# Optimization experiments

Hardware: AMD Instinct MI355X
Metric: run time of the kernel (lower is better)

Reference implementation:

```python
import jax, jax.numpy as jnp
import numpy as np
from functools import reduce
from itertools import combinations_with_replacement

ORDER = 2  # Volterra order (matches init_kwargs)


def setup_inputs() -> dict:
    key = jax.random.key(0)
    kx, ka, kw, kb = jax.random.split(key, 4)
    N, D, P = 8192, 256, 3  # nodes, feature dim (in_dim == out_dim), num adjacency powers
    X = jax.random.normal(kx, (N, D), dtype=jnp.float32)
    # dense adjacency powers, scaled so A @ X stays O(1)
    A = jax.random.normal(ka, (P, N, N), dtype=jnp.float32) / np.float32(np.sqrt(N))
    # projective_layers: order+1 Linear(in_dim, out_dim) -> stacked weights/biases
    W = jax.random.normal(kw, (ORDER + 1, D, D), dtype=jnp.float32) / np.float32(np.sqrt(D))
    b = jax.random.normal(kb, (ORDER + 1, D), dtype=jnp.float32) * np.float32(0.01)
    return {"X": X, "A": A, "W": W, "b": b}


def reference(X, A, W, b):
    P = A.shape[0]
    # mat_muls[p] = A_p @ X  -> [P, N, in_dim]
    mat_muls = jnp.einsum('pnm,md->pnd', A, X)
    # order-0 term: Linear_0(X)
    out = X @ W[0].T + b[0]
    for r in range(1, ORDER + 1):
        combos = list(combinations_with_replacement(range(P), r))
        # sum of Hadamard products over all index combinations of size r
        S = reduce(jnp.add,
                   [reduce(jnp.multiply, [mat_muls[i] for i in combo]) for combo in combos])
        # Linear_r applied per combination == (sum of products) @ W_r^T, but the
        # bias is added once PER combination in the original loop.
        out = out + S @ W[r].T + np.float32(len(combos)) * b[r]
    return jax.nn.relu(out)
```

## Files before the change

kernel.cpp:

```cpp
#include <hip/hip_runtime.h>
#include <stdint.h>

typedef __bf16 bf16x8 __attribute__((ext_vector_type(8)));
typedef float floatx4 __attribute__((ext_vector_type(4)));

#define MFMA16(a, b, c) __builtin_amdgcn_mfma_f32_16x16x32_bf16((a), (b), (c), 0, 0, 0)

__device__ __forceinline__ uint32_t pack2bf(float a, float b) {
  uint32_t ua = __builtin_bit_cast(uint32_t, a);
  uint32_t ub = __builtin_bit_cast(uint32_t, b);
  ua = (ua + 0x7fffu + ((ua >> 16) & 1u)) >> 16;
  ub = (ub + 0x7fffu + ((ub >> 16) & 1u)) >> 16;
  return ua | (ub << 16);
}

#define NN 8192
#define DD 256
#define PP 3

__global__ __launch_bounds__(256) void k_transpose_x(const float* __restrict__ X,
                                                     uint16_t* __restrict__ XT) {
  __shared__ float lds[32][260];
  const int n0 = blockIdx.x * 32;
  const int t = threadIdx.x;
#pragma unroll
  for (int j = 0; j < 8; ++j) {
    int idx = t + 256 * j;
    int n = idx >> 6;
    int c = (idx & 63) << 2;
    float4 v = *(const float4*)(X + (size_t)(n0 + n) * DD + c);
    lds[n][c] = v.x; lds[n][c + 1] = v.y; lds[n][c + 2] = v.z; lds[n][c + 3] = v.w;
  }
  __syncthreads();
  const int d = t;
  uint32_t w[16];
#pragma unroll
  for (int i = 0; i < 16; ++i) w[i] = pack2bf(lds[2 * i][d], lds[2 * i + 1][d]);
  uint4* dst = (uint4*)(XT + (size_t)d * NN + n0);
  dst[0] = make_uint4(w[0], w[1], w[2], w[3]);
  dst[1] = make_uint4(w[4], w[5], w[6], w[7]);
  dst[2] = make_uint4(w[8], w[9], w[10], w[11]);
  dst[3] = make_uint4(w[12], w[13], w[14], w[15]);
}

__global__ __launch_bounds__(256) void k_build_wcat(const float* __restrict__ W,
                                                    uint16_t* __restrict__ WcatT) {
  int idx = blockIdx.x * 256 + threadIdx.x;
  int o = idx * 4;
  int d = o / 768;
  int c = o - d * 768;
  int r = c >> 8;
  int e = c & 255;
  float4 v = *(const float4*)(W + (size_t)r * DD * DD + (size_t)d * DD + e);
  *(uint2*)(WcatT + o) = make_uint2(pack2bf(v.x, v.y), pack2bf(v.z, v.w));
}

__global__ __launch_bounds__(256) void k_gemm_ax(const float* __restrict__ A,
                                                 const uint16_t* __restrict__ XT,
                                                 float* __restrict__ M) {
  __shared__ uint16_t ldsA[4 * 64 * 8];
  __shared__ uint16_t ldsB[16 * 64 * 8];

  const int t = threadIdx.x;
  const int lane = t & 63;
  const int wid = t >> 6;
  const int wm = wid >> 1;
  const int wn = wid & 1;
  const int rt = blockIdx.x;
  const int p = blockIdx.y;

  const float* Ap = A + (size_t)p * NN * NN + (size_t)rt * 64 * NN;
  float* Mp = M + (size_t)p * NN * DD;

  const int arow = t >> 2;
  const int aq = t & 3;
  const float* aptr = Ap + (size_t)arow * NN + aq * 8;
  const int alds = (((arow >> 4) * 64) + ((aq << 4) | (arow & 15))) * 8;

  const uint16_t* xptr0;
  const uint16_t* xptr1;
  const uint16_t* xptr2;
  const uint16_t* xptr3;
  int xlds[4];
  {
    const uint16_t* tmp[4];
#pragma unroll
    for (int j = 0; j < 4; ++j) {
      int idx = t + 256 * j;
      int nl = idx >> 2;
      int q = idx & 3;
      tmp[j] = XT + (size_t)nl * NN + q * 8;
      xlds[j] = (((nl >> 4) * 64) + ((q << 4) | (nl & 15))) * 8;
    }
    xptr0 = tmp[0]; xptr1 = tmp[1]; xptr2 = tmp[2]; xptr3 = tmp[3];
  }

  floatx4 acc[2][8];
#pragma unroll
  for (int i = 0; i < 2; ++i)
#pragma unroll
    for (int j = 0; j < 8; ++j) acc[i][j] = (floatx4){0.f, 0.f, 0.f, 0.f};

  for (int k0 = 0; k0 < NN; k0 += 32) {
    float4 a0 = *(const float4*)(aptr);
    float4 a1 = *(const float4*)(aptr + 4);
    aptr += 32;
    uint4 xv0 = *(const uint4*)xptr0; xptr0 += 32;
    uint4 xv1 = *(const uint4*)xptr1; xptr1 += 32;
    uint4 xv2 = *(const uint4*)xptr2; xptr2 += 32;
    uint4 xv3 = *(const uint4*)xptr3; xptr3 += 32;

    __syncthreads();
    uint4 apk;
    apk.x = pack2bf(a0.x, a0.y);
    apk.y = pack2bf(a0.z, a0.w);
    apk.z = pack2bf(a1.x, a1.y);
    apk.w = pack2bf(a1.z, a1.w);
    *(uint4*)&ldsA[alds] = apk;
    *(uint4*)&ldsB[xlds[0]] = xv0;
    *(uint4*)&ldsB[xlds[1]] = xv1;
    *(uint4*)&ldsB[xlds[2]] = xv2;
    *(uint4*)&ldsB[xlds[3]] = xv3;
    __syncthreads();

    bf16x8 af0 = *(const bf16x8*)&ldsA[((wm * 2 + 0) * 64 + lane) * 8];
    bf16x8 af1 = *(const bf16x8*)&ldsA[((wm * 2 + 1) * 64 + lane) * 8];
#pragma unroll
    for (int j = 0; j < 8; ++j) {
      bf16x8 bf = *(const bf16x8*)&ldsB[((wn * 8 + j) * 64 + lane) * 8];
      acc[0][j] = MFMA16(af0, bf, acc[0][j]);
      acc[1][j] = MFMA16(af1, bf, acc[1][j]);
    }
  }

  const int quad = lane >> 4;
  const int cl = lane & 15;
#pragma unroll
  for (int i = 0; i < 2; ++i) {
    int rbase = rt * 64 + wm * 32 + i * 16 + quad * 4;
#pragma unroll
    for (int j = 0; j < 8; ++j) {
      int c = wn * 128 + j * 16 + cl;
#pragma unroll
      for (int r = 0; r < 4; ++r)
        Mp[(size_t)(rbase + r) * DD + c] = acc[i][j][r];
    }
  }
}

__global__ __launch_bounds__(256) void k_stage3(const float* __restrict__ X,
                                                const float* __restrict__ M,
                                                const uint16_t* __restrict__ WcatT,
                                                const float* __restrict__ b,
                                                float* __restrict__ out) {
  __shared__ uint16_t cat[48 * 64 * 8];
  const int row0 = blockIdx.x * 32;
  const int t = threadIdx.x;
  const float* M0 = M;
  const float* M1 = M + (size_t)NN * DD;
  const float* M2 = M + 2 * (size_t)NN * DD;

#pragma unroll
  for (int j = 0; j < 8; ++j) {
    int idx = t + 256 * j;
    int m = idx >> 6;
    int e = (idx & 63) << 2;
    size_t off = (size_t)(row0 + m) * DD + e;
    float4 xv = *(const float4*)(X + off);
    float4 a = *(const float4*)(M0 + off);
    float4 bb = *(const float4*)(M1 + off);
    float4 cc = *(const float4*)(M2 + off);
    float4 s1, s2;
    s1.x = a.x + bb.x + cc.x;
    s1.y = a.y + bb.y + cc.y;
    s1.z = a.z + bb.z + cc.z;
    s1.w = a.w + bb.w + cc.w;
    s2.x = a.x * a.x + bb.x * bb.x + cc.x * cc.x + a.x * bb.x + a.x * cc.x + bb.x * cc.x;
    s2.y = a.y * a.y + bb.y * bb.y + cc.y * cc.y + a.y * bb.y + a.y * cc.y + bb.y * cc.y;
    s2.z = a.z * a.z + bb.z * bb.z + cc.z * cc.z + a.z * bb.z + a.z * cc.z + bb.z * cc.z;
    s2.w = a.w * a.w + bb.w * bb.w + cc.w * cc.w + a.w * bb.w + a.w * cc.w + bb.w * cc.w;
#pragma unroll
    for (int part = 0; part < 3; ++part) {
      int k = part * 256 + e;
      int kt = k >> 5;
      int q = (k >> 3) & 3;
      int slot = (kt * 2 + (m >> 4)) * 64 + ((q << 4) | (m & 15));
      float4 v = (part == 0) ? xv : ((part == 1) ? s1 : s2);
      *(uint2*)&cat[slot * 8 + (k & 7)] = make_uint2(pack2bf(v.x, v.y), pack2bf(v.z, v.w));
    }
  }
  __syncthreads();

  const int lane = t & 63;
  const int w = t >> 6;
  const int cl = lane & 15;
  const int quad = lane >> 4;
  floatx4 acc[2][4];
#pragma unroll
  for (int i = 0; i < 2; ++i)
#pragma unroll
    for (int j = 0; j < 4; ++j) acc[i][j] = (floatx4){0.f, 0.f, 0.f, 0.f};

  for (int kt = 0; kt < 24; ++kt) {
    bf16x8 af0 = *(const bf16x8*)&cat[((kt * 2 + 0) * 64 + lane) * 8];
    bf16x8 af1 = *(const bf16x8*)&cat[((kt * 2 + 1) * 64 + lane) * 8];
#pragma unroll
    for (int j = 0; j < 4; ++j) {
      int d = w * 64 + j * 16 + cl;
      bf16x8 bv = *(const bf16x8*)(WcatT + (size_t)d * 768 + kt * 32 + quad * 8);
      acc[0][j] = MFMA16(af0, bv, acc[0][j]);
      acc[1][j] = MFMA16(af1, bv, acc[1][j]);
    }
  }

#pragma unroll
  for (int j = 0; j < 4; ++j) {
    int d = w * 64 + j * 16 + cl;
    float bias = b[d] + 3.0f * b[256 + d] + 6.0f * b[512 + d];
#pragma unroll
    for (int mt = 0; mt < 2; ++mt) {
      int rbase = row0 + mt * 16 + quad * 4;
#pragma unroll
      for (int r = 0; r < 4; ++r) {
        float v = acc[mt][j][r] + bias;
        out[(size_t)(rbase + r) * DD + d] = v > 0.f ? v : 0.f;
      }
    }
  }
}

extern "C" void kernel_launch(void* const* d_in, const int* in_sizes, int n_in,
                              void* d_out, int out_size, void* d_ws, size_t ws_size,
                              hipStream_t stream) {
  const float* X = (const float*)d_in[0];
  const float* A = (const float*)d_in[1];
  const float* W = (const float*)d_in[2];
  const float* b = (const float*)d_in[3];
  float* out = (float*)d_out;

  char* ws = (char*)d_ws;
  uint16_t* XT = (uint16_t*)ws;
  uint16_t* WcatT = (uint16_t*)(ws + 4194304);
  float* M = (float*)(ws + 4194304 + 393216);

  hipLaunchKernelGGL(k_transpose_x, dim3(NN / 32), dim3(256), 0, stream, X, XT);
  hipLaunchKernelGGL(k_build_wcat, dim3(192), dim3(256), 0, stream, W, WcatT);
  hipLaunchKernelGGL(k_gemm_ax, dim3(NN / 64, PP), dim3(256), 0, stream, A, XT, M);
  hipLaunchKernelGGL(k_stage3, dim3(NN / 32), dim3(256), 0, stream, X, M, WcatT, b, out);
}
```

Baseline: 1.247 ms.

## Pre-swizzle X into MFMA tile layout, load via global_load_lds, double K-step

The X transpose kernel now writes X in the exact per-lane MFMA fragment layout, tiled by 64-wide K blocks. The main GEMM copies these tiles straight into LDS with global_load_lds, skipping the register round-trip. The K step per iteration doubles from 32 to 64, which halves the barrier count and gives each A load 64 bytes per thread. The cost is larger LDS tiles, and there is still no double buffering, so loads and MFMA work remain serialized within a block.

```diff
diff --git a/kernel.cpp b/kernel.cpp
--- a/kernel.cpp
+++ b/kernel.cpp
@@ -14,33 +14,46 @@
   return ua | (ub << 16);
 }
 
+__device__ __forceinline__ void gload16(uint16_t* lds, const uint16_t* g) {
+  __builtin_amdgcn_global_load_lds(
+      (const __attribute__((address_space(1))) void*)g,
+      (__attribute__((address_space(3))) void*)lds, 16, 0, 0);
+}
+
 #define NN 8192
 #define DD 256
 #define PP 3
 
 __global__ __launch_bounds__(256) void k_transpose_x(const float* __restrict__ X,
-                                                     uint16_t* __restrict__ XT) {
-  __shared__ float lds[32][260];
-  const int n0 = blockIdx.x * 32;
+                                                     uint16_t* __restrict__ XTs) {
+  __shared__ float lds[64][133];
+  const int kt = blockIdx.x;
+  const int half = blockIdx.y;
   const int t = threadIdx.x;
 #pragma unroll
   for (int j = 0; j < 8; ++j) {
     int idx = t + 256 * j;
-    int n = idx >> 6;
-    int c = (idx & 63) << 2;
-    float4 v = *(const float4*)(X + (size_t)(n0 + n) * DD + c);
-    lds[n][c] = v.x; lds[n][c + 1] = v.y; lds[n][c + 2] = v.z; lds[n][c + 3] = v.w;
+    int m = idx >> 5;
+    int c = (idx & 31) << 2;
+    float4 v = *(const float4*)(X + (size_t)(kt * 64 + m) * DD + half * 128 + c);
+    lds[m][c] = v.x; lds[m][c + 1] = v.y; lds[m][c + 2] = v.z; lds[m][c + 3] = v.w;
   }
   __syncthreads();
-  const int d = t;
-  uint32_t w[16];
-#pragma unroll
-  for (int i = 0; i < 16; ++i) w[i] = pack2bf(lds[2 * i][d], lds[2 * i + 1][d]);
-  uint4* dst = (uint4*)(XT + (size_t)d * NN + n0);
-  dst[0] = make_uint4(w[0], w[1], w[2], w[3]);
-  dst[1] = make_uint4(w[4], w[5], w[6], w[7]);
-  dst[2] = make_uint4(w[8], w[9], w[10], w[11]);
-  dst[3] = make_uint4(w[12], w[13], w[14], w[15]);
+#pragma unroll
+  for (int j = 0; j < 4; ++j) {
+    int slot = t + 256 * j;
+    int tl = slot >> 6;
+    int lane = slot & 63;
+    int ks = tl >> 3, ntl = tl & 7;
+    int q = lane >> 4, dl = ntl * 16 + (lane & 15);
+    int kb = ks * 32 + q * 8;
+    uint32_t w0 = pack2bf(lds[kb + 0][dl], lds[kb + 1][dl]);
+    uint32_t w1 = pack2bf(lds[kb + 2][dl], lds[kb + 3][dl]);
+    uint32_t w2 = pack2bf(lds[kb + 4][dl], lds[kb + 5][dl]);
+    uint32_t w3 = pack2bf(lds[kb + 6][dl], lds[kb + 7][dl]);
+    int tile = ks * 16 + half * 8 + ntl;
+    *(uint4*)(XTs + (((size_t)kt * 32 + tile) * 64 + lane) * 8) = make_uint4(w0, w1, w2, w3);
+  }
 }
 
 __global__ __launch_bounds__(256) void k_build_wcat(const float* __restrict__ W,
@@ -56,10 +69,10 @@
 }
 
 __global__ __launch_bounds__(256) void k_gemm_ax(const float* __restrict__ A,
-                                                 const uint16_t* __restrict__ XT,
+                                                 const uint16_t* __restrict__ XTs,
                                                  float* __restrict__ M) {
-  __shared__ uint16_t ldsA[4 * 64 * 8];
-  __shared__ uint16_t ldsB[16 * 64 * 8];
+  __shared__ uint16_t ldsA[8 * 64 * 8];
+  __shared__ uint16_t ldsB[32 * 64 * 8];
 
   const int t = threadIdx.x;
   const int lane = t & 63;
@@ -73,27 +86,10 @@
   float* Mp = M + (size_t)p * NN * DD;
 
   const int arow = t >> 2;
-  const int aq = t & 3;
-  const float* aptr = Ap + (size_t)arow * NN + aq * 8;
-  const int alds = (((arow >> 4) * 64) + ((aq << 4) | (arow & 15))) * 8;
-
-  const uint16_t* xptr0;
-  const uint16_t* xptr1;
-  const uint16_t* xptr2;
-  const uint16_t* xptr3;
-  int xlds[4];
-  {
-    const uint16_t* tmp[4];
-#pragma unroll
-    for (int j = 0; j < 4; ++j) {
-      int idx = t + 256 * j;
-      int nl = idx >> 2;
-      int q = idx & 3;
-      tmp[j] = XT + (size_t)nl * NN + q * 8;
-      xlds[j] = (((nl >> 4) * 64) + ((q << 4) | (nl & 15))) * 8;
-    }
-    xptr0 = tmp[0]; xptr1 = tmp[1]; xptr2 = tmp[2]; xptr3 = tmp[3];
-  }
+  const int a8 = t & 3;
+  const float4* asrc = (const float4*)(Ap + (size_t)arow * NN + a8 * 16);
+  const int alds0 = ((((a8 >> 1) * 4 + (arow >> 4)) * 64) +
+                     ((((a8 & 1) * 2) << 4) | (arow & 15))) * 8;
 
   floatx4 acc[2][8];
 #pragma unroll
@@ -101,35 +97,37 @@
 #pragma unroll
     for (int j = 0; j < 8; ++j) acc[i][j] = (floatx4){0.f, 0.f, 0.f, 0.f};
 
-  for (int k0 = 0; k0 < NN; k0 += 32) {
-    float4 a0 = *(const float4*)(aptr);
-    float4 a1 = *(const float4*)(aptr + 4);
-    aptr += 32;
-    uint4 xv0 = *(const uint4*)xptr0; xptr0 += 32;
-    uint4 xv1 = *(const uint4*)xptr1; xptr1 += 32;
-    uint4 xv2 = *(const uint4*)xptr2; xptr2 += 32;
-    uint4 xv3 = *(const uint4*)xptr3; xptr3 += 32;
+  for (int kt = 0; kt < 128; ++kt) {
+    float4 a0 = asrc[0], a1 = asrc[1], a2 = asrc[2], a3 = asrc[3];
+    asrc += 16;
 
     __syncthreads();
-    uint4 apk;
-    apk.x = pack2bf(a0.x, a0.y);
-    apk.y = pack2bf(a0.z, a0.w);
-    apk.z = pack2bf(a1.x, a1.y);
-    apk.w = pack2bf(a1.z, a1.w);
-    *(uint4*)&ldsA[alds] = apk;
-    *(uint4*)&ldsB[xlds[0]] = xv0;
-    *(uint4*)&ldsB[xlds[1]] = xv1;
-    *(uint4*)&ldsB[xlds[2]] = xv2;
-    *(uint4*)&ldsB[xlds[3]] = xv3;
+
+    const uint16_t* xb = XTs + ((size_t)kt * 32 + wid * 8) * 512 + lane * 8;
+#pragma unroll
+    for (int i = 0; i < 8; ++i)
+      gload16(&ldsB[(wid * 8 + i) * 512], xb + i * 512);
+
+    uint4 w;
+    w.x = pack2bf(a0.x, a0.y); w.y = pack2bf(a0.z, a0.w);
+    w.z = pack2bf(a1.x, a1.y); w.w = pack2bf(a1.z, a1.w);
+    *(uint4*)&ldsA[alds0] = w;
+    w.x = pack2bf(a2.x, a2.y); w.y = pack2bf(a2.z, a2.w);
+    w.z = pack2bf(a3.x, a3.y); w.w = pack2bf(a3.z, a3.w);
+    *(uint4*)&ldsA[alds0 + 128] = w;
+
     __syncthreads();
 
-    bf16x8 af0 = *(const bf16x8*)&ldsA[((wm * 2 + 0) * 64 + lane) * 8];
-    bf16x8 af1 = *(const bf16x8*)&ldsA[((wm * 2 + 1) * 64 + lane) * 8];
-#pragma unroll
-    for (int j = 0; j < 8; ++j) {
-      bf16x8 bf = *(const bf16x8*)&ldsB[((wn * 8 + j) * 64 + lane) * 8];
-      acc[0][j] = MFMA16(af0, bf, acc[0][j]);
-      acc[1][j] = MFMA16(af1, bf, acc[1][j]);
+#pragma unroll
+    for (int ks = 0; ks < 2; ++ks) {
+      bf16x8 af0 = *(const bf16x8*)&ldsA[((ks * 4 + wm * 2 + 0) * 64 + lane) * 8];
+      bf16x8 af1 = *(const bf16x8*)&ldsA[((ks * 4 + wm * 2 + 1) * 64 + lane) * 8];
+#pragma unroll
+      for (int j = 0; j < 8; ++j) {
+        bf16x8 bf = *(const bf16x8*)&ldsB[((ks * 16 + wn * 8 + j) * 64 + lane) * 8];
+        acc[0][j] = MFMA16(af0, bf, acc[0][j]);
+        acc[1][j] = MFMA16(af1, bf, acc[1][j]);
+      }
     }
   }
 
@@ -243,7 +241,7 @@
   uint16_t* WcatT = (uint16_t*)(ws + 4194304);
   float* M = (float*)(ws + 4194304 + 393216);
 
-  hipLaunchKernelGGL(k_transpose_x, dim3(NN / 32), dim3(256), 0, stream, X, XT);
+  hipLaunchKernelGGL(k_transpose_x, dim3(128, 2), dim3(256), 0, stream, X, XT);
   hipLaunchKernelGGL(k_build_wcat, dim3(192), dim3(256), 0, stream, W, WcatT);
   hipLaunchKernelGGL(k_gemm_ax, dim3(NN / 64, PP), dim3(256), 0, stream, A, XT, M);
   hipLaunchKernelGGL(k_stage3, dim3(NN / 32), dim3(256), 0, stream, X, M, WcatT, b, out);
```

Result: faster. 1.209 ms (-3.0%).
